# Kernel tuning notes

Hardware: AMD Instinct MI355X
Metric: run time of the kernel (lower is better)

The kernel has to match this reference:

```python
import jax, jax.numpy as jnp
import numpy as np

N, CIN, COUT, K, CSTYLE, H, W = 8, 512, 512, 3, 512, 64, 64
EPS = 1e-8
SQRT2 = 2.0 ** 0.5


def setup_inputs() -> dict:
    key = jax.random.key(0)
    ks = jax.random.split(key, 5)
    return {
        "x": jax.random.normal(ks[0], (N, CIN, H, W), jnp.float32),
        "style": jax.random.normal(ks[1], (N, CSTYLE), jnp.float32),
        "noise": jax.random.normal(ks[2], (N, 1, H, W), jnp.float32),
        "conv_weight": jax.random.normal(ks[3], (1, COUT, CIN, K, K), jnp.float32),
        "mod_weight": jax.random.normal(ks[4], (CIN, CSTYLE), jnp.float32) / np.float32(np.sqrt(CSTYLE)),
        "mod_bias": jnp.ones((CIN,), jnp.float32),
        "noise_weight": jnp.zeros((1,), jnp.float32),
        "act_bias": jnp.zeros((COUT,), jnp.float32),
    }


def reference(x, style, noise, conv_weight, mod_weight, mod_bias, noise_weight, act_bias):
    n = x.shape[0]
    # style modulation: linear(style) -> per-sample per-in-channel scale (style_bias=0)
    s = style @ mod_weight.T + mod_bias                       # (n, cin)
    # modulate shared weight (1, cout, cin, k, k) -> (n, cout, cin, k, k)
    w = conv_weight * s[:, None, :, None, None]
    # demodulate
    demod = jax.lax.rsqrt(jnp.sum(w * w, axis=(2, 3, 4)) + EPS)  # (n, cout)
    w = w * demod[:, :, None, None, None]
    # grouped conv: groups = batch
    w = w.reshape(n * COUT, CIN, K, K)
    xg = x.reshape(1, n * CIN, H, W)
    out = jax.lax.conv_general_dilated(
        xg, w,
        window_strides=(1, 1),
        padding=[(K // 2, K // 2), (K // 2, K // 2)],
        dimension_numbers=("NCHW", "OIHW", "NCHW"),
        feature_group_count=n,
    )
    out = out.reshape(n, COUT, H, W) * SQRT2
    # noise injection (scalar weight, broadcast noise)
    out = out + noise_weight[0] * noise
    # fused bias + leaky relu (slope 0.2)
    out = jax.nn.leaky_relu(out + act_bias[None, :, None, None], negative_slope=0.2)
    return out
```

## Files before the change

kernel.cpp:

```cpp
#include <hip/hip_runtime.h>
#include <hip/hip_bf16.h>
#include <stdint.h>


typedef __attribute__((ext_vector_type(8))) short short8;
typedef __attribute__((ext_vector_type(4))) float f32x4;
typedef __attribute__((ext_vector_type(4))) unsigned int uint4v;
typedef __attribute__((ext_vector_type(2))) unsigned int uint2v;

__device__ __forceinline__ unsigned short f2bf(float f) {
  unsigned u = __builtin_bit_cast(unsigned, f);
  u += 0x7FFFu + ((u >> 16) & 1u);
  return (unsigned short)(u >> 16);
}

__device__ __forceinline__ void g2l16(const void* g, void* l) {
  __builtin_amdgcn_global_load_lds(
      (const __attribute__((address_space(1))) void*)g,
      (__attribute__((address_space(3))) void*)l, 16, 0, 0);
}

__global__ void k_prep(const float* __restrict__ style, const float* __restrict__ mw,
                       const float* __restrict__ mb, const float* __restrict__ cw,
                       const float* __restrict__ x, float* __restrict__ demod_g,
                       unsigned short* __restrict__ Xp, unsigned short* __restrict__ Wt) {
  __shared__ __align__(16) char smem[74240];
  int t = threadIdx.x;
  int b = blockIdx.x;
  if (b < 512) {
    int n = b >> 6, h = b & 63;
    short* ldsx = (short*)smem;
    float* sxf  = (float*)(smem + 69632);
    float* stl  = (float*)(smem + 71680);
    stl[t] = style[n * 512 + t];
    stl[t + 256] = style[n * 512 + 256 + t];
    __syncthreads();
    {
      int lane = t & 63, wv = t >> 6;
      int g = lane >> 4, l = lane & 15;
#pragma unroll 2
      for (int cr = 0; cr < 32; ++cr) {
        int ci = wv * 128 + cr * 4 + g;
        const float* mr = mw + (size_t)ci * 512;
        float sum = 0.f;
#pragma unroll
        for (int it = 0; it < 8; ++it) {
          f32x4 a = *(const f32x4*)(mr + l * 4 + it * 64);
          f32x4 sv = *(const f32x4*)(stl + l * 4 + it * 64);
          sum += a.x * sv.x + a.y * sv.y + a.z * sv.z + a.w * sv.w;
        }
        sum += __shfl_xor(sum, 1, 64);
        sum += __shfl_xor(sum, 2, 64);
        sum += __shfl_xor(sum, 4, 64);
        sum += __shfl_xor(sum, 8, 64);
        if (l == 0) sxf[ci] = sum + mb[ci];
      }
    }
    __syncthreads();
    {
      int g = t >> 5, l5 = t & 31;
      int co = h * 8 + g;
      const float* cwb = cw + (size_t)co * 4608;
      float sum = 0.f;
#pragma unroll
      for (int i = 0; i < 16; ++i) {
        int ci = l5 + i * 32;
        const float* p = cwb + ci * 9;
        float a = 0.f;
#pragma unroll
        for (int j = 0; j < 9; ++j) a += p[j] * p[j];
        float sv = sxf[ci];
        sum += sv * sv * a;
      }
#pragma unroll
      for (int off = 16; off; off >>= 1) sum += __shfl_xor(sum, off, 64);
      if (l5 == 0)
        demod_g[n * 512 + co] = rsqrtf(sum + 1e-8f) * 1.41421356237309515f;
    }
    const float* xb = x + ((size_t)n * 512) * 4096 + h * 64;
#pragma unroll
    for (int i = 0; i < 32; ++i) {
      int L = t + i * 256;
      int ci = L >> 4, q = L & 15;
      f32x4 v = *(const f32x4*)(xb + (size_t)ci * 4096 + q * 4);
      float sv = sxf[ci];
      uint2v o;
      o.x = f2bf(v.x * sv) | ((unsigned)f2bf(v.y * sv) << 16);
      o.y = f2bf(v.z * sv) | ((unsigned)f2bf(v.w * sv) << 16);
      *(uint2v*)(ldsx + ci * 68 + q * 4) = o;
    }
    __syncthreads();
    unsigned short* nb = Xp + (size_t)n * 2230272 + (size_t)(h + 1) * 33792;
#pragma unroll
    for (int r = 0; r < 16; ++r) {
      int u = t + r * 256;
      int cig = u >> 6, col = u & 63;
      unsigned v[8];
#pragma unroll
      for (int j = 0; j < 8; ++j)
        v[j] = (unsigned short)ldsx[(cig * 8 + j) * 68 + col];
      uint4v o;
      o.x = v[0] | (v[1] << 16);
      o.y = v[2] | (v[3] << 16);
      o.z = v[4] | (v[5] << 16);
      o.w = v[6] | (v[7] << 16);
      *(uint4v*)(nb + ((size_t)cig * 66 + col + 1) * 8) = o;
    }
  } else if (b < 640) {
    int bb = b - 512;
    int cb = bb >> 4, kb = bb & 15;
    float* ldsf = (float*)smem;
#pragma unroll
    for (int i = 0; i < 72; ++i) {
      int idx = t + i * 256;
      int seg = idx / 288, off = idx - seg * 288;
      ldsf[seg * 289 + off] = cw[(size_t)(cb * 64 + seg) * 4608 + kb * 288 + off];
    }
    __syncthreads();
    unsigned short* ob = Wt + (size_t)(cb * 16 + kb) * 18432;
#pragma unroll
    for (int i = 0; i < 9; ++i) {
      int c = t + i * 256;
      int m = c & 15, lhi = (c >> 4) & 3, mt = (c >> 6) & 3, tap = c >> 8;
      int co_rel = mt * 16 + m;
      unsigned v[8];
#pragma unroll
      for (int j = 0; j < 8; ++j)
        v[j] = f2bf(ldsf[co_rel * 289 + (lhi * 8 + j) * 9 + tap]);
      uint4v o;
      o.x = v[0] | (v[1] << 16);
      o.y = v[2] | (v[3] << 16);
      o.z = v[4] | (v[5] << 16);
      o.w = v[6] | (v[7] << 16);
      *(uint4v*)(ob + (size_t)c * 8) = o;
    }
  } else {
    int bb = b - 640;
    int n = bb / 17, part = bb % 17;
    uint4v z = (uint4v){0u, 0u, 0u, 0u};
    unsigned short* base = Xp + (size_t)n * 2230272;
#pragma unroll
    for (int i = 0; i < 4; ++i) {
      int id = part * 1024 + i * 256 + t;
      if (id < 16640) {
        size_t off;
        if (id < 8448) {
          int row = (id < 4224) ? 0 : 65;
          int c = id - ((id < 4224) ? 0 : 4224);
          off = (size_t)row * 33792 + (size_t)c * 8;
        } else {
          int id2 = id - 8448;
          int row = 1 + (id2 >> 7);
          int rem = id2 & 127;
          int klhi = rem >> 1;
          int col = (rem & 1) ? 65 : 0;
          off = (size_t)row * 33792 + ((size_t)klhi * 66 + col) * 8;
        }
        *(uint4v*)(base + off) = z;
      }
    }
  }
}

__global__ void __launch_bounds__(256, 2) k_conv(
    const unsigned short* __restrict__ Wt, const unsigned short* __restrict__ Xp,
    const float* __restrict__ demod, const float* __restrict__ noise,
    const float* __restrict__ nw_p, const float* __restrict__ act_bias,
    float* __restrict__ out) {
  __shared__ short lds_a[18432];
  __shared__ short lds_x[22528];
  int t = threadIdx.x;
  int r0 = blockIdx.x * 8;
  int cb = blockIdx.y;
  int n = blockIdx.z;
  int lane = t & 63, wv = t >> 6;
  int l15 = lane & 15, lhi = lane >> 4;

  const unsigned short* abase = Wt + (size_t)cb * 16 * 18432;
  const unsigned short* xbase = Xp + (size_t)n * 2230272;
  int xoffg[11];
#pragma unroll
  for (int j = 0; j < 11; ++j) {
    int c = j * 256 + t;
    int r = c / 264, rc = c - r * 264;
    int off = (r0 + r) * 33792 + rc * 8;
    if (c >= 2640) off = 0;
    xoffg[j] = off;
  }

  f32x4 acc[4][8];
#pragma unroll
  for (int a = 0; a < 4; ++a)
#pragma unroll
    for (int bq = 0; bq < 8; ++bq) acc[a][bq] = (f32x4){0.f, 0.f, 0.f, 0.f};

  const int aoff = lhi * 128 + l15 * 8;
  const int xoffb = lhi * 528 + (wv * 16 + l15) * 8;

  for (int kb = 0; kb < 16; ++kb) {
    __syncthreads();
    const char* ab = (const char*)(abase + (size_t)kb * 18432);
#pragma unroll
    for (int i = 0; i < 9; ++i)
      g2l16(ab + i * 4096 + t * 16, (char*)lds_a + i * 4096 + t * 16);
#pragma unroll
    for (int j = 0; j < 11; ++j)
      g2l16(xbase + xoffg[j] + kb * 2112, (char*)lds_x + j * 4096 + t * 16);
    __syncthreads();

#pragma unroll
    for (int dw = 0; dw < 3; ++dw) {
      short8 bf[10];
#pragma unroll
      for (int rr = 0; rr < 10; ++rr)
        bf[rr] = *(const short8*)(lds_x + rr * 2112 + dw * 8 + xoffb);
#pragma unroll
      for (int dh = 0; dh < 3; ++dh) {
#pragma unroll
        for (int mt = 0; mt < 4; ++mt) {
          short8 af = *(const short8*)(lds_a + (dh * 3 + dw) * 2048 + mt * 512 + aoff);
#pragma unroll
          for (int ri = 0; ri < 8; ++ri)
            acc[mt][ri] =
                __builtin_amdgcn_mfma_f32_16x16x32_bf16(af, bf[ri + dh], acc[mt][ri], 0, 0, 0);
        }
      }
    }
  }

  float nw = nw_p[0];
  int col = wv * 16 + l15;
  float nz[8];
#pragma unroll
  for (int ri = 0; ri < 8; ++ri)
    nz[ri] = nw * noise[((size_t)n * 64 + r0 + ri) * 64 + col];
#pragma unroll
  for (int mt = 0; mt < 4; ++mt) {
    f32x4 dm4 = *(const f32x4*)(demod + n * 512 + cb * 64 + mt * 16 + lhi * 4);
#pragma unroll
    for (int c = 0; c < 4; ++c) {
      int co = cb * 64 + mt * 16 + lhi * 4 + c;
      float ab2 = act_bias[co];
      float dm = dm4[c];
#pragma unroll
      for (int ri = 0; ri < 8; ++ri) {
        float v = dm * acc[mt][ri][c] + nz[ri] + ab2;
        v = v > 0.f ? v : 0.2f * v;
        out[(((size_t)n * 512 + co) * 64 + (r0 + ri)) * 64 + col] = v;
      }
    }
  }
}

extern "C" void kernel_launch(void* const* d_in, const int* in_sizes, int n_in,
                              void* d_out, int out_size, void* d_ws, size_t ws_size,
                              hipStream_t stream) {
  const float* x     = (const float*)d_in[0];
  const float* style = (const float*)d_in[1];
  const float* noise = (const float*)d_in[2];
  const float* cw    = (const float*)d_in[3];
  const float* mw    = (const float*)d_in[4];
  const float* mb    = (const float*)d_in[5];
  const float* nw    = (const float*)d_in[6];
  const float* ab    = (const float*)d_in[7];
  float* out = (float*)d_out;

  char* ws = (char*)d_ws;
  float* demod  = (float*)(ws + 16384);
  unsigned short* Wt = (unsigned short*)(ws + 1081344);
  unsigned short* Xp = (unsigned short*)(ws + 5799936);

  k_prep<<<776, 256, 0, stream>>>(style, mw, mb, cw, x, demod, Xp, Wt);
  k_conv<<<dim3(8, 8, 8), 256, 0, stream>>>(Wt, Xp, demod, noise, nw, ab, out);
}
```

Measured before the change: 280.7 us.

## Fuse input modulation and bf16 packing into conv, compute demod per block

The prep kernel no longer builds a padded, modulated bf16 copy of x in workspace. The conv kernel now reads fp32 x directly each k-block, scales it by the style vector, converts and packs it into LDS, and handles the zero halo itself. Demodulation is split: a prep pass stores per-(co,ci) squared weight sums, and each conv block reduces them with its sample's style. This removes the intermediate Xp write and read, at the cost of strided scalar global loads and conversion work inside the conv main loop. That work is not overlapped with the MFMAs and is repeated across the 8 output-channel blocks that share each input tile.

After: 412.2 us. +46.8%, slower.

```diff
diff --git a/kernel.cpp b/kernel.cpp
--- a/kernel.cpp
+++ b/kernel.cpp
@@ -6,7 +6,6 @@
 typedef __attribute__((ext_vector_type(8))) short short8;
 typedef __attribute__((ext_vector_type(4))) float f32x4;
 typedef __attribute__((ext_vector_type(4))) unsigned int uint4v;
-typedef __attribute__((ext_vector_type(2))) unsigned int uint2v;
 
 __device__ __forceinline__ unsigned short f2bf(float f) {
   unsigned u = __builtin_bit_cast(unsigned, f);
@@ -20,94 +19,40 @@
       (__attribute__((address_space(3))) void*)l, 16, 0, 0);
 }
 
-__global__ void k_prep(const float* __restrict__ style, const float* __restrict__ mw,
-                       const float* __restrict__ mb, const float* __restrict__ cw,
-                       const float* __restrict__ x, float* __restrict__ demod_g,
-                       unsigned short* __restrict__ Xp, unsigned short* __restrict__ Wt) {
+__global__ void k_wprep(const float* __restrict__ style, const float* __restrict__ mw,
+                        const float* __restrict__ mb, const float* __restrict__ cw,
+                        float* __restrict__ s_g, float* __restrict__ wsq,
+                        unsigned short* __restrict__ Wt) {
   __shared__ __align__(16) char smem[74240];
   int t = threadIdx.x;
   int b = blockIdx.x;
-  if (b < 512) {
-    int n = b >> 6, h = b & 63;
-    short* ldsx = (short*)smem;
-    float* sxf  = (float*)(smem + 69632);
-    float* stl  = (float*)(smem + 71680);
+  if (b < 8) {
+    int n = b;
+    float* stl = (float*)smem;
     stl[t] = style[n * 512 + t];
     stl[t + 256] = style[n * 512 + 256 + t];
     __syncthreads();
-    {
-      int lane = t & 63, wv = t >> 6;
-      int g = lane >> 4, l = lane & 15;
+    int lane = t & 63, wv = t >> 6;
+    int g = lane >> 4, l = lane & 15;
 #pragma unroll 2
-      for (int cr = 0; cr < 32; ++cr) {
-        int ci = wv * 128 + cr * 4 + g;
-        const float* mr = mw + (size_t)ci * 512;
-        float sum = 0.f;
-#pragma unroll
-        for (int it = 0; it < 8; ++it) {
-          f32x4 a = *(const f32x4*)(mr + l * 4 + it * 64);
-          f32x4 sv = *(const f32x4*)(stl + l * 4 + it * 64);
-          sum += a.x * sv.x + a.y * sv.y + a.z * sv.z + a.w * sv.w;
-        }
-        sum += __shfl_xor(sum, 1, 64);
-        sum += __shfl_xor(sum, 2, 64);
-        sum += __shfl_xor(sum, 4, 64);
-        sum += __shfl_xor(sum, 8, 64);
-        if (l == 0) sxf[ci] = sum + mb[ci];
-      }
-    }
-    __syncthreads();
-    {
-      int g = t >> 5, l5 = t & 31;
-      int co = h * 8 + g;
-      const float* cwb = cw + (size_t)co * 4608;
+    for (int cr = 0; cr < 32; ++cr) {
+      int ci = wv * 128 + cr * 4 + g;
+      const float* mr = mw + (size_t)ci * 512;
       float sum = 0.f;
 #pragma unroll
-      for (int i = 0; i < 16; ++i) {
-        int ci = l5 + i * 32;
-        const float* p = cwb + ci * 9;
-        float a = 0.f;
-#pragma unroll
-        for (int j = 0; j < 9; ++j) a += p[j] * p[j];
-        float sv = sxf[ci];
-        sum += sv * sv * a;
-      }
-#pragma unroll
-      for (int off = 16; off; off >>= 1) sum += __shfl_xor(sum, off, 64);
-      if (l5 == 0)
-        demod_g[n * 512 + co] = rsqrtf(sum + 1e-8f) * 1.41421356237309515f;
-    }
-    const float* xb = x + ((size_t)n * 512) * 4096 + h * 64;
-#pragma unroll
-    for (int i = 0; i < 32; ++i) {
-      int L = t + i * 256;
-      int ci = L >> 4, q = L & 15;
-      f32x4 v = *(const f32x4*)(xb + (size_t)ci * 4096 + q * 4);
-      float sv = sxf[ci];
-      uint2v o;
-      o.x = f2bf(v.x * sv) | ((unsigned)f2bf(v.y * sv) << 16);
-      o.y = f2bf(v.z * sv) | ((unsigned)f2bf(v.w * sv) << 16);
-      *(uint2v*)(ldsx + ci * 68 + q * 4) = o;
-    }
-    __syncthreads();
-    unsigned short* nb = Xp + (size_t)n * 2230272 + (size_t)(h + 1) * 33792;
-#pragma unroll
-    for (int r = 0; r < 16; ++r) {
-      int u = t + r * 256;
-      int cig = u >> 6, col = u & 63;
-      unsigned v[8];
-#pragma unroll
-      for (int j = 0; j < 8; ++j)
-        v[j] = (unsigned short)ldsx[(cig * 8 + j) * 68 + col];
-      uint4v o;
-      o.x = v[0] | (v[1] << 16);
-      o.y = v[2] | (v[3] << 16);
-      o.z = v[4] | (v[5] << 16);
-      o.w = v[6] | (v[7] << 16);
-      *(uint4v*)(nb + ((size_t)cig * 66 + col + 1) * 8) = o;
-    }
-  } else if (b < 640) {
-    int bb = b - 512;
+      for (int it = 0; it < 8; ++it) {
+        f32x4 a = *(const f32x4*)(mr + l * 4 + it * 64);
+        f32x4 sv = *(const f32x4*)(stl + l * 4 + it * 64);
+        sum += a.x * sv.x + a.y * sv.y + a.z * sv.z + a.w * sv.w;
+      }
+      sum += __shfl_xor(sum, 1, 64);
+      sum += __shfl_xor(sum, 2, 64);
+      sum += __shfl_xor(sum, 4, 64);
+      sum += __shfl_xor(sum, 8, 64);
+      if (l == 0) s_g[n * 512 + ci] = sum + mb[ci];
+    }
+  } else if (b < 136) {
+    int bb = b - 8;
     int cb = bb >> 4, kb = bb & 15;
     float* ldsf = (float*)smem;
 #pragma unroll
@@ -135,67 +80,73 @@
       *(uint4v*)(ob + (size_t)c * 8) = o;
     }
   } else {
-    int bb = b - 640;
-    int n = bb / 17, part = bb % 17;
-    uint4v z = (uint4v){0u, 0u, 0u, 0u};
-    unsigned short* base = Xp + (size_t)n * 2230272;
-#pragma unroll
-    for (int i = 0; i < 4; ++i) {
-      int id = part * 1024 + i * 256 + t;
-      if (id < 16640) {
-        size_t off;
-        if (id < 8448) {
-          int row = (id < 4224) ? 0 : 65;
-          int c = id - ((id < 4224) ? 0 : 4224);
-          off = (size_t)row * 33792 + (size_t)c * 8;
-        } else {
-          int id2 = id - 8448;
-          int row = 1 + (id2 >> 7);
-          int rem = id2 & 127;
-          int klhi = rem >> 1;
-          int col = (rem & 1) ? 65 : 0;
-          off = (size_t)row * 33792 + ((size_t)klhi * 66 + col) * 8;
-        }
-        *(uint4v*)(base + off) = z;
-      }
+    int base = (b - 136) * 2048;
+#pragma unroll
+    for (int u = 0; u < 8; ++u) {
+      int id = base + u * 256 + t;
+      const float* p = cw + (size_t)id * 9;
+      float a = 0.f;
+#pragma unroll
+      for (int j = 0; j < 9; ++j) a += p[j] * p[j];
+      wsq[id] = a;
     }
   }
 }
 
 __global__ void __launch_bounds__(256, 2) k_conv(
-    const unsigned short* __restrict__ Wt, const unsigned short* __restrict__ Xp,
-    const float* __restrict__ demod, const float* __restrict__ noise,
-    const float* __restrict__ nw_p, const float* __restrict__ act_bias,
-    float* __restrict__ out) {
-  __shared__ short lds_a[18432];
-  __shared__ short lds_x[22528];
+    const unsigned short* __restrict__ Wt, const float* __restrict__ x,
+    const float* __restrict__ s_g, const float* __restrict__ wsq,
+    const float* __restrict__ noise, const float* __restrict__ nw_p,
+    const float* __restrict__ act_bias, float* __restrict__ out) {
+  __shared__ __align__(16) char smem[81408];
+  short* lds_a = (short*)smem;
+  short* lds_x = (short*)(smem + 36864);
+  float* sxf   = (float*)(smem + 79104);
+  float* demf  = (float*)(smem + 81152);
   int t = threadIdx.x;
   int r0 = blockIdx.x * 8;
   int cb = blockIdx.y;
   int n = blockIdx.z;
   int lane = t & 63, wv = t >> 6;
-  int l15 = lane & 15, lhi = lane >> 4;
-
+  int l15 = lane & 15, lhi4 = lane >> 4;
+
+  sxf[t] = s_g[n * 512 + t];
+  sxf[t + 256] = s_g[n * 512 + 256 + t];
+  __syncthreads();
+  {
+    int g = t >> 5, l5 = t & 31;
+    const float* wb = wsq + (size_t)(cb * 64) * 512;
+#pragma unroll
+    for (int q = 0; q < 8; ++q) {
+      int coi = g * 8 + q;
+      float sum = 0.f;
+#pragma unroll
+      for (int i = 0; i < 4; ++i) {
+        int c4 = l5 * 4 + i * 128;
+        f32x4 w4 = *(const f32x4*)(wb + (size_t)coi * 512 + c4);
+        f32x4 s4 = *(const f32x4*)(sxf + c4);
+        sum += s4.x * s4.x * w4.x + s4.y * s4.y * w4.y +
+               s4.z * s4.z * w4.z + s4.w * s4.w * w4.w;
+      }
+      sum += __shfl_xor(sum, 1, 64);
+      sum += __shfl_xor(sum, 2, 64);
+      sum += __shfl_xor(sum, 4, 64);
+      sum += __shfl_xor(sum, 8, 64);
+      sum += __shfl_xor(sum, 16, 64);
+      if (l5 == 0) demf[coi] = rsqrtf(sum + 1e-8f) * 1.41421356237309515f;
+    }
+  }
+
+  f32x4 acc[4][8];
+#pragma unroll
+  for (int a = 0; a < 4; ++a)
+#pragma unroll
+    for (int bq = 0; bq < 8; ++bq) acc[a][bq] = (f32x4){0.f, 0.f, 0.f, 0.f};
+
+  const int aoff = lhi4 * 128 + l15 * 8;
+  const int xoffb = lhi4 * 528 + (wv * 16 + l15) * 8;
   const unsigned short* abase = Wt + (size_t)cb * 16 * 18432;
-  const unsigned short* xbase = Xp + (size_t)n * 2230272;
-  int xoffg[11];
-#pragma unroll
-  for (int j = 0; j < 11; ++j) {
-    int c = j * 256 + t;
-    int r = c / 264, rc = c - r * 264;
-    int off = (r0 + r) * 33792 + rc * 8;
-    if (c >= 2640) off = 0;
-    xoffg[j] = off;
-  }
-
-  f32x4 acc[4][8];
-#pragma unroll
-  for (int a = 0; a < 4; ++a)
-#pragma unroll
-    for (int bq = 0; bq < 8; ++bq) acc[a][bq] = (f32x4){0.f, 0.f, 0.f, 0.f};
-
-  const int aoff = lhi * 128 + l15 * 8;
-  const int xoffb = lhi * 528 + (wv * 16 + l15) * 8;
+  const float* xn = x + (size_t)n * 512 * 4096;
 
   for (int kb = 0; kb < 16; ++kb) {
     __syncthreads();
@@ -203,9 +154,53 @@
 #pragma unroll
     for (int i = 0; i < 9; ++i)
       g2l16(ab + i * 4096 + t * 16, (char*)lds_a + i * 4096 + t * 16);
-#pragma unroll
-    for (int j = 0; j < 11; ++j)
-      g2l16(xbase + xoffg[j] + kb * 2112, (char*)lds_x + j * 4096 + t * 16);
+
+    {
+      int ci0 = kb * 32 + wv * 8;
+      f32x4 sA = *(const f32x4*)(sxf + ci0);
+      f32x4 sB = *(const f32x4*)(sxf + ci0 + 4);
+      float cm = (lane >= 1) ? 1.f : 0.f;
+      int xcc = lane - 1; if (xcc < 0) xcc = 0;
+#pragma unroll
+      for (int p = 0; p < 10; ++p) {
+        int off = p * 2112 + wv * 528 + lane * 8;
+        int xr = r0 + p - 1;
+        if ((unsigned)xr < 64u) {
+          const float* bp = xn + (size_t)ci0 * 4096 + xr * 64 + xcc;
+          float v0 = bp[0], v1 = bp[4096], v2 = bp[8192], v3 = bp[12288];
+          float v4 = bp[16384], v5 = bp[20480], v6 = bp[24576], v7 = bp[28672];
+          uint4v o;
+          o.x = f2bf(v0 * sA.x * cm) | ((unsigned)f2bf(v1 * sA.y * cm) << 16);
+          o.y = f2bf(v2 * sA.z * cm) | ((unsigned)f2bf(v3 * sA.w * cm) << 16);
+          o.z = f2bf(v4 * sB.x * cm) | ((unsigned)f2bf(v5 * sB.y * cm) << 16);
+          o.w = f2bf(v6 * sB.z * cm) | ((unsigned)f2bf(v7 * sB.w * cm) << 16);
+          *(uint4v*)(lds_x + off) = o;
+        } else {
+          *(uint4v*)(lds_x + off) = (uint4v){0u, 0u, 0u, 0u};
+        }
+      }
+      if (t < 80) {
+        int row = t >> 3, lhi = (t >> 1) & 3, c_lds = 64 + (t & 1);
+        int off = row * 2112 + lhi * 528 + c_lds * 8;
+        int xr = r0 + row - 1;
+        if ((unsigned)xr < 64u && c_lds == 64) {
+          int ci0b = kb * 32 + lhi * 8;
+          f32x4 sC = *(const f32x4*)(sxf + ci0b);
+          f32x4 sD = *(const f32x4*)(sxf + ci0b + 4);
+          const float* bp = xn + (size_t)ci0b * 4096 + xr * 64 + 63;
+          float v0 = bp[0], v1 = bp[4096], v2 = bp[8192], v3 = bp[12288];
+          float v4 = bp[16384], v5 = bp[20480], v6 = bp[24576], v7 = bp[28672];
+          uint4v o;
+          o.x = f2bf(v0 * sC.x) | ((unsigned)f2bf(v1 * sC.y) << 16);
+          o.y = f2bf(v2 * sC.z) | ((unsigned)f2bf(v3 * sC.w) << 16);
+          o.z = f2bf(v4 * sD.x) | ((unsigned)f2bf(v5 * sD.y) << 16);
+          o.w = f2bf(v6 * sD.z) | ((unsigned)f2bf(v7 * sD.w) << 16);
+          *(uint4v*)(lds_x + off) = o;
+        } else {
+          *(uint4v*)(lds_x + off) = (uint4v){0u, 0u, 0u, 0u};
+        }
+      }
+    }
     __syncthreads();
 
 #pragma unroll
@@ -236,10 +231,10 @@
     nz[ri] = nw * noise[((size_t)n * 64 + r0 + ri) * 64 + col];
 #pragma unroll
   for (int mt = 0; mt < 4; ++mt) {
-    f32x4 dm4 = *(const f32x4*)(demod + n * 512 + cb * 64 + mt * 16 + lhi * 4);
+    f32x4 dm4 = *(const f32x4*)(demf + mt * 16 + lhi4 * 4);
 #pragma unroll
     for (int c = 0; c < 4; ++c) {
-      int co = cb * 64 + mt * 16 + lhi * 4 + c;
+      int co = cb * 64 + mt * 16 + lhi4 * 4 + c;
       float ab2 = act_bias[co];
       float dm = dm4[c];
 #pragma unroll
@@ -266,10 +261,10 @@
   float* out = (float*)d_out;
 
   char* ws = (char*)d_ws;
-  float* demod  = (float*)(ws + 16384);
+  float* s_g  = (float*)ws;
+  float* wsq  = (float*)(ws + 32768);
   unsigned short* Wt = (unsigned short*)(ws + 1081344);
-  unsigned short* Xp = (unsigned short*)(ws + 5799936);
-
-  k_prep<<<776, 256, 0, stream>>>(style, mw, mb, cw, x, demod, Xp, Wt);
-  k_conv<<<dim3(8, 8, 8), 256, 0, stream>>>(Wt, Xp, demod, noise, nw, ab, out);
-}
+
+  k_wprep<<<264, 256, 0, stream>>>(style, mw, mb, cw, s_g, wsq, Wt);
+  k_conv<<<dim3(8, 8, 8), 256, 0, stream>>>(Wt, x, s_g, wsq, noise, nw, ab, out);
+}
```

## Split prep work into smaller blocks and move demodulation into conv kernel

Applied to the files above, without the earlier changes.

The prep kernel now splits each x-row block into two channel halves with half the LDS, adds separate blocks for style modulation and per-(co,ci) squared weight sums, and processes the weight transpose in four passes with a smaller LDS buffer. Demodulation is removed from prep and recomputed at the start of each conv block from the precomputed style scales and weight-square sums. The aim is higher occupancy and less redundant per-block work in prep, which previously recomputed style modulation and demod in 512 blocks with a large LDS footprint. The cost is extra demod work and a larger shared allocation in every conv block, plus the style projection still being repeated per half-block.

Measured after the change: 295.4 us. 5.2% more time.

```diff
diff --git a/kernel.cpp b/kernel.cpp
--- a/kernel.cpp
+++ b/kernel.cpp
@@ -20,18 +20,22 @@
       (__attribute__((address_space(3))) void*)l, 16, 0, 0);
 }
 
-__global__ void k_prep(const float* __restrict__ style, const float* __restrict__ mw,
-                       const float* __restrict__ mb, const float* __restrict__ cw,
-                       const float* __restrict__ x, float* __restrict__ demod_g,
-                       unsigned short* __restrict__ Xp, unsigned short* __restrict__ Wt) {
-  __shared__ __align__(16) char smem[74240];
+__global__ void __launch_bounds__(256, 4) k_prep(
+    const float* __restrict__ style, const float* __restrict__ mw,
+    const float* __restrict__ mb, const float* __restrict__ cw,
+    const float* __restrict__ x, float* __restrict__ s_g,
+    float* __restrict__ wsq, unsigned short* __restrict__ Xp,
+    unsigned short* __restrict__ Wt) {
+  __shared__ __align__(16) char smem[37888];
   int t = threadIdx.x;
   int b = blockIdx.x;
-  if (b < 512) {
-    int n = b >> 6, h = b & 63;
+  if (b < 1024) {
+    int n = b >> 7;
+    int rest = b & 127;
+    int h = rest >> 1, half = rest & 1;
     short* ldsx = (short*)smem;
-    float* sxf  = (float*)(smem + 69632);
-    float* stl  = (float*)(smem + 71680);
+    float* sxf  = (float*)(smem + 34816);
+    float* stl  = (float*)(smem + 35840);
     stl[t] = style[n * 512 + t];
     stl[t + 256] = style[n * 512 + 256 + t];
     __syncthreads();
@@ -39,8 +43,9 @@
       int lane = t & 63, wv = t >> 6;
       int g = lane >> 4, l = lane & 15;
 #pragma unroll 2
-      for (int cr = 0; cr < 32; ++cr) {
-        int ci = wv * 128 + cr * 4 + g;
+      for (int cr = 0; cr < 16; ++cr) {
+        int cil = wv * 64 + cr * 4 + g;
+        int ci = half * 256 + cil;
         const float* mr = mw + (size_t)ci * 512;
         float sum = 0.f;
 #pragma unroll
@@ -53,52 +58,33 @@
         sum += __shfl_xor(sum, 2, 64);
         sum += __shfl_xor(sum, 4, 64);
         sum += __shfl_xor(sum, 8, 64);
-        if (l == 0) sxf[ci] = sum + mb[ci];
-      }
-    }
-    __syncthreads();
-    {
-      int g = t >> 5, l5 = t & 31;
-      int co = h * 8 + g;
-      const float* cwb = cw + (size_t)co * 4608;
-      float sum = 0.f;
-#pragma unroll
-      for (int i = 0; i < 16; ++i) {
-        int ci = l5 + i * 32;
-        const float* p = cwb + ci * 9;
-        float a = 0.f;
-#pragma unroll
-        for (int j = 0; j < 9; ++j) a += p[j] * p[j];
-        float sv = sxf[ci];
-        sum += sv * sv * a;
-      }
-#pragma unroll
-      for (int off = 16; off; off >>= 1) sum += __shfl_xor(sum, off, 64);
-      if (l5 == 0)
-        demod_g[n * 512 + co] = rsqrtf(sum + 1e-8f) * 1.41421356237309515f;
-    }
-    const float* xb = x + ((size_t)n * 512) * 4096 + h * 64;
-#pragma unroll
-    for (int i = 0; i < 32; ++i) {
+        if (l == 0) sxf[cil] = sum + mb[ci];
+      }
+    }
+    __syncthreads();
+    const float* xb = x + ((size_t)(n * 512 + half * 256)) * 4096 + h * 64;
+#pragma unroll
+    for (int i = 0; i < 16; ++i) {
       int L = t + i * 256;
-      int ci = L >> 4, q = L & 15;
-      f32x4 v = *(const f32x4*)(xb + (size_t)ci * 4096 + q * 4);
-      float sv = sxf[ci];
+      int cil = L >> 4, q = L & 15;
+      f32x4 v = *(const f32x4*)(xb + (size_t)cil * 4096 + q * 4);
+      float sv = sxf[cil];
       uint2v o;
       o.x = f2bf(v.x * sv) | ((unsigned)f2bf(v.y * sv) << 16);
       o.y = f2bf(v.z * sv) | ((unsigned)f2bf(v.w * sv) << 16);
-      *(uint2v*)(ldsx + ci * 68 + q * 4) = o;
+      *(uint2v*)(ldsx + cil * 68 + q * 4) = o;
     }
     __syncthreads();
     unsigned short* nb = Xp + (size_t)n * 2230272 + (size_t)(h + 1) * 33792;
 #pragma unroll
-    for (int r = 0; r < 16; ++r) {
+    for (int r = 0; r < 8; ++r) {
       int u = t + r * 256;
-      int cig = u >> 6, col = u & 63;
+      int cigl = u >> 6, col = u & 63;
+      int cig = half * 32 + cigl;
       unsigned v[8];
 #pragma unroll
       for (int j = 0; j < 8; ++j)
-        v[j] = (unsigned short)ldsx[(cig * 8 + j) * 68 + col];
+        v[j] = (unsigned short)ldsx[(cigl * 8 + j) * 68 + col];
       uint4v o;
       o.x = v[0] | (v[1] << 16);
       o.y = v[2] | (v[3] << 16);
@@ -106,36 +92,79 @@
       o.w = v[6] | (v[7] << 16);
       *(uint4v*)(nb + ((size_t)cig * 66 + col + 1) * 8) = o;
     }
-  } else if (b < 640) {
-    int bb = b - 512;
+  } else if (b < 1032) {
+    int n = b - 1024;
+    float* stl = (float*)smem;
+    stl[t] = style[n * 512 + t];
+    stl[t + 256] = style[n * 512 + 256 + t];
+    __syncthreads();
+    int lane = t & 63, wv = t >> 6;
+    int g = lane >> 4, l = lane & 15;
+#pragma unroll 2
+    for (int cr = 0; cr < 32; ++cr) {
+      int ci = wv * 128 + cr * 4 + g;
+      const float* mr = mw + (size_t)ci * 512;
+      float sum = 0.f;
+#pragma unroll
+      for (int it = 0; it < 8; ++it) {
+        f32x4 a = *(const f32x4*)(mr + l * 4 + it * 64);
+        f32x4 sv = *(const f32x4*)(stl + l * 4 + it * 64);
+        sum += a.x * sv.x + a.y * sv.y + a.z * sv.z + a.w * sv.w;
+      }
+      sum += __shfl_xor(sum, 1, 64);
+      sum += __shfl_xor(sum, 2, 64);
+      sum += __shfl_xor(sum, 4, 64);
+      sum += __shfl_xor(sum, 8, 64);
+      if (l == 0) s_g[n * 512 + ci] = sum + mb[ci];
+    }
+  } else if (b < 1160) {
+    int bb = b - 1032;
     int cb = bb >> 4, kb = bb & 15;
     float* ldsf = (float*)smem;
-#pragma unroll
-    for (int i = 0; i < 72; ++i) {
-      int idx = t + i * 256;
-      int seg = idx / 288, off = idx - seg * 288;
-      ldsf[seg * 289 + off] = cw[(size_t)(cb * 64 + seg) * 4608 + kb * 288 + off];
-    }
-    __syncthreads();
     unsigned short* ob = Wt + (size_t)(cb * 16 + kb) * 18432;
 #pragma unroll
-    for (int i = 0; i < 9; ++i) {
-      int c = t + i * 256;
-      int m = c & 15, lhi = (c >> 4) & 3, mt = (c >> 6) & 3, tap = c >> 8;
-      int co_rel = mt * 16 + m;
-      unsigned v[8];
-#pragma unroll
-      for (int j = 0; j < 8; ++j)
-        v[j] = f2bf(ldsf[co_rel * 289 + (lhi * 8 + j) * 9 + tap]);
-      uint4v o;
-      o.x = v[0] | (v[1] << 16);
-      o.y = v[2] | (v[3] << 16);
-      o.z = v[4] | (v[5] << 16);
-      o.w = v[6] | (v[7] << 16);
-      *(uint4v*)(ob + (size_t)c * 8) = o;
+    for (int p = 0; p < 4; ++p) {
+      __syncthreads();
+#pragma unroll
+      for (int i = 0; i < 18; ++i) {
+        int idx = t + i * 256;
+        int segl = idx / 288, off = idx - segl * 288;
+        ldsf[segl * 289 + off] =
+            cw[(size_t)(cb * 64 + p * 16 + segl) * 4608 + kb * 288 + off];
+      }
+      __syncthreads();
+#pragma unroll
+      for (int i = 0; i < 3; ++i) {
+        int e = t + i * 256;
+        if (e < 576) {
+          int tap = e >> 6, lhi = (e >> 4) & 3, m = e & 15;
+          int c = tap * 256 + p * 64 + lhi * 16 + m;
+          unsigned v[8];
+#pragma unroll
+          for (int j = 0; j < 8; ++j)
+            v[j] = f2bf(ldsf[m * 289 + (lhi * 8 + j) * 9 + tap]);
+          uint4v o;
+          o.x = v[0] | (v[1] << 16);
+          o.y = v[2] | (v[3] << 16);
+          o.z = v[4] | (v[5] << 16);
+          o.w = v[6] | (v[7] << 16);
+          *(uint4v*)(ob + (size_t)c * 8) = o;
+        }
+      }
+    }
+  } else if (b < 1288) {
+    int base = (b - 1160) * 2048;
+#pragma unroll
+    for (int u = 0; u < 8; ++u) {
+      int id = base + u * 256 + t;
+      const float* p = cw + (size_t)id * 9;
+      float a = 0.f;
+#pragma unroll
+      for (int j = 0; j < 9; ++j) a += p[j] * p[j];
+      wsq[id] = a;
     }
   } else {
-    int bb = b - 640;
+    int bb = b - 1288;
     int n = bb / 17, part = bb % 17;
     uint4v z = (uint4v){0u, 0u, 0u, 0u};
     unsigned short* base = Xp + (size_t)n * 2230272;
@@ -164,17 +193,52 @@
 
 __global__ void __launch_bounds__(256, 2) k_conv(
     const unsigned short* __restrict__ Wt, const unsigned short* __restrict__ Xp,
-    const float* __restrict__ demod, const float* __restrict__ noise,
-    const float* __restrict__ nw_p, const float* __restrict__ act_bias,
-    float* __restrict__ out) {
-  __shared__ short lds_a[18432];
-  __shared__ short lds_x[22528];
+    const float* __restrict__ s_g, const float* __restrict__ wsq,
+    const float* __restrict__ noise, const float* __restrict__ nw_p,
+    const float* __restrict__ act_bias, float* __restrict__ out) {
+  __shared__ __align__(16) char smem[81920];
+  short* lds_a = (short*)smem;
+  short* lds_x = (short*)(smem + 36864);
   int t = threadIdx.x;
   int r0 = blockIdx.x * 8;
   int cb = blockIdx.y;
   int n = blockIdx.z;
   int lane = t & 63, wv = t >> 6;
-  int l15 = lane & 15, lhi = lane >> 4;
+  int l15 = lane & 15, lhi4 = lane >> 4;
+
+  f32x4 dmreg[4];
+  {
+    float* sxf  = (float*)(smem + 36864);
+    float* demf = (float*)(smem + 36864 + 2048);
+    sxf[t] = s_g[n * 512 + t];
+    sxf[t + 256] = s_g[n * 512 + 256 + t];
+    __syncthreads();
+    int g = t >> 5, l5 = t & 31;
+    const float* wb = wsq + (size_t)(cb * 64) * 512;
+#pragma unroll
+    for (int q = 0; q < 8; ++q) {
+      int coi = g * 8 + q;
+      float sum = 0.f;
+#pragma unroll
+      for (int i = 0; i < 4; ++i) {
+        int c4 = l5 * 4 + i * 128;
+        f32x4 w4 = *(const f32x4*)(wb + (size_t)coi * 512 + c4);
+        f32x4 s4 = *(const f32x4*)(sxf + c4);
+        sum += s4.x * s4.x * w4.x + s4.y * s4.y * w4.y +
+               s4.z * s4.z * w4.z + s4.w * s4.w * w4.w;
+      }
+      sum += __shfl_xor(sum, 1, 64);
+      sum += __shfl_xor(sum, 2, 64);
+      sum += __shfl_xor(sum, 4, 64);
+      sum += __shfl_xor(sum, 8, 64);
+      sum += __shfl_xor(sum, 16, 64);
+      if (l5 == 0) demf[coi] = rsqrtf(sum + 1e-8f) * 1.41421356237309515f;
+    }
+    __syncthreads();
+#pragma unroll
+    for (int mt = 0; mt < 4; ++mt)
+      dmreg[mt] = *(const f32x4*)(demf + mt * 16 + lhi4 * 4);
+  }
 
   const unsigned short* abase = Wt + (size_t)cb * 16 * 18432;
   const unsigned short* xbase = Xp + (size_t)n * 2230272;
@@ -194,8 +258,8 @@
 #pragma unroll
     for (int bq = 0; bq < 8; ++bq) acc[a][bq] = (f32x4){0.f, 0.f, 0.f, 0.f};
 
-  const int aoff = lhi * 128 + l15 * 8;
-  const int xoffb = lhi * 528 + (wv * 16 + l15) * 8;
+  const int aoff = lhi4 * 128 + l15 * 8;
+  const int xoffb = lhi4 * 528 + (wv * 16 + l15) * 8;
 
   for (int kb = 0; kb < 16; ++kb) {
     __syncthreads();
@@ -236,10 +300,10 @@
     nz[ri] = nw * noise[((size_t)n * 64 + r0 + ri) * 64 + col];
 #pragma unroll
   for (int mt = 0; mt < 4; ++mt) {
-    f32x4 dm4 = *(const f32x4*)(demod + n * 512 + cb * 64 + mt * 16 + lhi * 4);
+    f32x4 dm4 = dmreg[mt];
 #pragma unroll
     for (int c = 0; c < 4; ++c) {
-      int co = cb * 64 + mt * 16 + lhi * 4 + c;
+      int co = cb * 64 + mt * 16 + lhi4 * 4 + c;
       float ab2 = act_bias[co];
       float dm = dm4[c];
 #pragma unroll
@@ -266,10 +330,11 @@
   float* out = (float*)d_out;
 
   char* ws = (char*)d_ws;
-  float* demod  = (float*)(ws + 16384);
+  float* s_g  = (float*)ws;
+  float* wsq  = (float*)(ws + 32768);
   unsigned short* Wt = (unsigned short*)(ws + 1081344);
   unsigned short* Xp = (unsigned short*)(ws + 5799936);
 
-  k_prep<<<776, 256, 0, stream>>>(style, mw, mb, cw, x, demod, Xp, Wt);
-  k_conv<<<dim3(8, 8, 8), 256, 0, stream>>>(Wt, Xp, demod, noise, nw, ab, out);
-}
+  k_prep<<<1424, 256, 0, stream>>>(style, mw, mb, cw, x, s_g, wsq, Xp, Wt);
+  k_conv<<<dim3(8, 8, 8), 256, 0, stream>>>(Wt, Xp, s_g, wsq, noise, nw, ab, out);
+}
```
